# Kernel optimization log

Hardware: AMD Instinct MI355X
Metric: run time of the kernel (lower is better)

Reference implementation:

```python
import jax, jax.numpy as jnp
import numpy as np

N_NODES = 50000


def gcn_conv(x, edge_index, W, b):
    """PyG GCNConv: add self-loops, symmetric deg^{-1/2} norm, W then aggregate."""
    n = x.shape[0]
    loops = jnp.arange(n, dtype=edge_index.dtype)
    src = jnp.concatenate([edge_index[0], loops])  # message sources
    dst = jnp.concatenate([edge_index[1], loops])  # aggregation targets
    h = x @ W  # [N, out_dim] -- transform before gather (PyG order)
    deg = jax.ops.segment_sum(jnp.ones_like(dst, dtype=h.dtype), dst, num_segments=n)
    dinv = jnp.where(deg > 0, jax.lax.rsqrt(jnp.maximum(deg, 1.0)), 0.0)
    norm = dinv[src] * dinv[dst]  # [E+N]
    msg = h[src] * norm[:, None]  # gather + normalize
    out = jax.ops.segment_sum(msg, dst, num_segments=n)  # scatter-add
    return out + b


def setup_inputs() -> dict:
    key = jax.random.key(0)
    k1, k2, k3, k4, k5 = jax.random.split(key, 5)
    N, E, D_IN, D_H, D_OUT = N_NODES, 800000, 128, 256, 16
    x = jax.random.normal(k1, (N, D_IN), dtype=jnp.float32)
    edge_index = jax.random.randint(k2, (2, E), 0, N, dtype=jnp.int64)
    s1 = 1.0 / np.sqrt(D_IN)
    s2 = 1.0 / np.sqrt(D_H)
    W1 = jax.random.uniform(k3, (D_IN, D_H), jnp.float32, -s1, s1)
    b1 = jnp.zeros((D_H,), jnp.float32)
    W2 = jax.random.uniform(k4, (D_H, D_OUT), jnp.float32, -s2, s2)
    b2 = jnp.zeros((D_OUT,), jnp.float32)
    return {"x": x, "edge_index": edge_index, "W1": W1, "b1": b1, "W2": W2, "b2": b2}


def reference(x, edge_index, W1, b1, W2, b2):
    h = jax.nn.relu(gcn_conv(x, edge_index, W1, b1))
    # dropout is identity in eval mode
    logits = gcn_conv(h, edge_index, W2, b2)
    return jax.nn.log_softmax(logits, axis=-1)
```

## Files before the change

### kernel.cpp

```cpp
#include <hip/hip_runtime.h>
#include <math.h>

typedef unsigned int uint;
typedef unsigned short u16;
typedef short short8 __attribute__((ext_vector_type(8)));
typedef float floatx4 __attribute__((ext_vector_type(4)));

union U4S8 { uint4 u; short8 s; };

#define CAPC   64
#define BPB    2048
#define BINCAP 4608


__device__ __forceinline__ float blo(uint u) { return __uint_as_float(u << 16); }
__device__ __forceinline__ float bhi(uint u) { return __uint_as_float(u & 0xffff0000u); }
__device__ __forceinline__ uint pack_bf16(float a, float b) {
    uint ua = __float_as_uint(a), ub = __float_as_uint(b);
    ua = (ua + 0x7fffu + ((ua >> 16) & 1u)) >> 16;
    ub = (ub + 0x7fffu + ((ub >> 16) & 1u)) >> 16;
    return ua | (ub << 16);
}
__device__ __forceinline__ unsigned short rb16(float f) {
    uint u = __float_as_uint(f);
    return (unsigned short)((u + 0x7fffu + ((u >> 16) & 1u)) >> 16);
}
__device__ __forceinline__ int us(short v) { return (int)(unsigned short)v; }

__device__ __forceinline__ int xcd_id() {
    return (int)(__builtin_amdgcn_s_getreg((3 << 11) | 20) & 7);
}


__global__ __launch_bounds__(256) void k_bucket_direct(
    const int* __restrict__ ei, int E, int nblk,
    uint* __restrict__ binctr8, uint* __restrict__ ebin,
    const float* __restrict__ W1, const float* __restrict__ W2,
    uint* __restrict__ W1t, uint* __restrict__ W2t)
{
    __shared__ uint hist[256];
    __shared__ uint off[256];
    int blk = blockIdx.x, tid = threadIdx.x;
    if (blk < nblk) {
        int xcd = xcd_id();
        hist[tid] = 0;
        __syncthreads();
        int base = blk * BPB, end = min(base + BPB, E);
        for (int i = base + tid; i < end; i += 256)
            atomicAdd(&hist[ei[E + i] >> 8], 1u);
        __syncthreads();
        uint h = hist[tid];
        off[tid] = h ? atomicAdd(&binctr8[xcd * 256 + tid], h) : 0u;
        hist[tid] = 0;
        __syncthreads();
        for (int i = base + tid; i < end; i += 256) {
            int sv = ei[i], tv = ei[E + i];
            int bin = tv >> 8;
            uint local = atomicAdd(&hist[bin], 1u);
            uint pos = off[bin] + local;
            if (pos < BINCAP)
                ebin[(size_t)(xcd * 256 + bin) * BINCAP + pos] =
                    ((uint)tv << 16) | (uint)sv;
        }
    } else {
        int i = (blk - nblk) * 256 + tid;
        if (i < 16384) {
            int nn = i >> 6, kd = i & 63;
            W1t[i] = pack_bf16(W1[(size_t)(2 * kd) * 256 + nn], W1[(size_t)(2 * kd + 1) * 256 + nn]);
        } else if (i < 16384 + 2048) {
            int j = i - 16384;
            int o = j >> 7, kd = j & 127;
            W2t[j] = pack_bf16(W2[(size_t)(2 * kd) * 16 + o], W2[(size_t)(2 * kd + 1) * 16 + o]);
        }
    }
}


__global__ __launch_bounds__(256) void k_binbucket(
    const uint* __restrict__ ebin, const uint* __restrict__ binctr8,
    u16* __restrict__ colc, int* __restrict__ degc, float* __restrict__ dinv, int n)
{
    __shared__ uint lbw[64 * 32];
    __shared__ uint lc[64];
    u16* lb = (u16*)lbw;
    int blk = blockIdx.x, tid = threadIdx.x;
    int p = blk >> 2, q = blk & 3;
    int node0 = (p << 8) + (q << 6);

    if (tid < 64) lc[tid] = 0;
    __syncthreads();

    #pragma unroll
    for (int x = 0; x < 8; ++x) {
        uint m = min(binctr8[x * 256 + p], (uint)BINCAP);
        size_t base = (size_t)(x * 256 + p) * BINCAP;
        for (uint i = tid; i < m; i += 256) {
            uint e = ebin[base + i];
            int tl = (int)((e >> 16) & 255u);
            if ((tl >> 6) == q) {
                uint c = atomicAdd(&lc[tl & 63], 1u);
                if (c < (uint)CAPC) lb[(tl & 63) * CAPC + c] = (u16)(e & 0xffffu);
            }
        }
    }
    __syncthreads();

    if (tid < 64) {
        int node = node0 + tid;
        if (node < n) {
            degc[node] = (int)min(lc[tid], (uint)CAPC);
            dinv[node] = rsqrtf((float)lc[tid] + 1.0f);
        }
    }
    uint* colw = (uint*)colc;
    for (int idx = tid; idx < 64 * 32; idx += 256) {
        int nd = node0 + (idx >> 5);
        if (nd < n) colw[(size_t)nd * 32 + (idx & 31)] = lbw[idx];
    }
}


__global__ void k_scale_cast(const float* __restrict__ dinv,
                             const float2* __restrict__ x2,
                             uint* __restrict__ xsb, int total) {
    int j = blockIdx.x * 256 + threadIdx.x;
    if (j >= total) return;
    int row = j >> 6;
    float di = dinv[row];
    float2 v = x2[j];
    xsb[j] = pack_bf16(v.x * di, v.y * di);
}


__global__ __launch_bounds__(256) void k_agg_csr128(
    const int* __restrict__ degc, const u16* __restrict__ colc,
    const float* __restrict__ dinv, const uint* __restrict__ xsb,
    uint* __restrict__ outb, int n)
{
    int node = (blockIdx.x * 256 + threadIdx.x) >> 6;
    int lane = threadIdx.x & 63;
    if (node >= n) return;
    float di = dinv[node];
    int deg = __builtin_amdgcn_readfirstlane(min(degc[node], CAPC));
    const u16* bucket = colc + (size_t)node * CAPC;
    uint u = xsb[(size_t)node * 64 + lane];
    float ax = blo(u), ay = bhi(u);
    for (int j = 0; j < deg; j += 16) {
        U4S8 b0, b1;
        b0.u = *(const uint4*)&bucket[j];
        b1.u = *(const uint4*)&bucket[j + 8];
        uint uu[16];
        #pragma unroll
        for (int k = 0; k < 8; ++k)
            uu[k] = (j + k < deg) ? xsb[(size_t)us(b0.s[k]) * 64 + lane] : 0u;
        #pragma unroll
        for (int k = 0; k < 8; ++k)
            uu[8 + k] = (j + 8 + k < deg) ? xsb[(size_t)us(b1.s[k]) * 64 + lane] : 0u;
        #pragma unroll
        for (int k = 0; k < 16; ++k) { ax += blo(uu[k]); ay += bhi(uu[k]); }
    }
    outb[(size_t)node * 64 + lane] = pack_bf16(ax * di, ay * di);
}


__global__ __launch_bounds__(256) void k_gemm_mfma(
    const uint* __restrict__ Ab,
    const uint* __restrict__ W1t,
    const float* __restrict__ b1,
    const uint* __restrict__ W2t,
    const float* __restrict__ dinv,
    float* __restrict__ H2, int M)
{
    __shared__ uint Alds[64 * 68];
    __shared__ uint Hlds[64 * 132];

    const int t    = threadIdx.x;
    const int mb   = blockIdx.x * 64;
    const int wv   = t >> 6;
    const int lane = t & 63;
    const int c    = lane & 15;
    const int q    = lane >> 4;

    #pragma unroll
    for (int it = 0; it < 4; ++it) {
        int i = it * 256 + t;
        int r = i >> 4, cc = i & 15;
        int gr = mb + r;
        uint4 v = make_uint4(0u, 0u, 0u, 0u);
        if (gr < M) v = ((const uint4*)Ab)[(size_t)gr * 16 + cc];
        *(uint4*)&Alds[r * 68 + cc * 4] = v;
    }
    __syncthreads();

    floatx4 acc[4][4];
    #pragma unroll
    for (int i = 0; i < 4; ++i)
        #pragma unroll
        for (int jj = 0; jj < 4; ++jj) acc[i][jj] = (floatx4)0.f;

    #pragma unroll
    for (int kk = 0; kk < 4; ++kk) {
        U4S8 af[4];
        #pragma unroll
        for (int mt = 0; mt < 4; ++mt)
            af[mt].u = *(const uint4*)&Alds[(mt * 16 + c) * 68 + kk * 16 + q * 4];
        #pragma unroll
        for (int nt = 0; nt < 4; ++nt) {
            int n = wv * 64 + nt * 16 + c;
            U4S8 bf;
            bf.u = ((const uint4*)W1t)[(size_t)n * 16 + kk * 4 + q];
            #pragma unroll
            for (int mt = 0; mt < 4; ++mt)
                acc[mt][nt] = __builtin_amdgcn_mfma_f32_16x16x32_bf16(
                    af[mt].s, bf.s, acc[mt][nt], 0, 0, 0);
        }
    }

    float b1v[4];
    #pragma unroll
    for (int nt = 0; nt < 4; ++nt) b1v[nt] = b1[wv * 64 + nt * 16 + c];

    unsigned short* hs = (unsigned short*)Hlds;
    #pragma unroll
    for (int mt = 0; mt < 4; ++mt)
        #pragma unroll
        for (int nt = 0; nt < 4; ++nt)
            #pragma unroll
            for (int r = 0; r < 4; ++r) {
                float hv = fmaxf(acc[mt][nt][r] + b1v[nt], 0.f);
                int row = mt * 16 + q * 4 + r;
                int colc2 = wv * 64 + nt * 16 + c;
                hs[row * 264 + colc2] = rb16(hv);
            }
    __syncthreads();

    floatx4 acc2 = (floatx4)0.f;
    #pragma unroll
    for (int kk = 0; kk < 8; ++kk) {
        U4S8 av, bv;
        av.u = *(const uint4*)&Hlds[(wv * 16 + c) * 132 + kk * 16 + q * 4];
        bv.u = ((const uint4*)W2t)[(size_t)c * 32 + kk * 4 + q];
        acc2 = __builtin_amdgcn_mfma_f32_16x16x32_bf16(av.s, bv.s, acc2, 0, 0, 0);
    }
    #pragma unroll
    for (int r = 0; r < 4; ++r) {
        int gr = mb + wv * 16 + q * 4 + r;
        if (gr < M) H2[(size_t)gr * 16 + c] = acc2[r] * dinv[gr];
    }
}


__global__ __launch_bounds__(256) void k_agg_csr16_lsm(
    const int* __restrict__ degc, const u16* __restrict__ colc,
    const float* __restrict__ dinv, const float* __restrict__ h2s,
    const float* __restrict__ b2, float* __restrict__ out, int n)
{
    int node = (blockIdx.x * 256 + threadIdx.x) >> 4;
    int lane = threadIdx.x & 15;
    if (node >= n) return;
    float di = dinv[node];
    int deg = min(degc[node], CAPC);
    const u16* bucket = colc + (size_t)node * CAPC;
    float acc = h2s[(size_t)node * 16 + lane];
    for (int j = 0; j < deg; j += 16) {
        U4S8 b0, b1;
        b0.u = *(const uint4*)&bucket[j];
        b1.u = *(const uint4*)&bucket[j + 8];
        float vv[16];
        #pragma unroll
        for (int k = 0; k < 8; ++k)
            vv[k] = (j + k < deg) ? h2s[(size_t)us(b0.s[k]) * 16 + lane] : 0.f;
        #pragma unroll
        for (int k = 0; k < 8; ++k)
            vv[8 + k] = (j + 8 + k < deg) ? h2s[(size_t)us(b1.s[k]) * 16 + lane] : 0.f;
        #pragma unroll
        for (int k = 0; k < 16; ++k) acc += vv[k];
    }
    acc = acc * di + b2[lane];
    float m = acc;
    #pragma unroll
    for (int msk = 1; msk < 16; msk <<= 1) m = fmaxf(m, __shfl_xor(m, msk, 16));
    float ex = __expf(acc - m);
    float ssum = ex;
    #pragma unroll
    for (int msk = 1; msk < 16; msk <<= 1) ssum += __shfl_xor(ssum, msk, 16);
    out[(size_t)node * 16 + lane] = acc - m - __logf(ssum);
}


extern "C" void kernel_launch(void* const* d_in, const int* in_sizes, int n_in,
                              void* d_out, int out_size, void* d_ws, size_t ws_size,
                              hipStream_t stream) {
    const float* x  = (const float*)d_in[0];
    const int*   ei = (const int*)d_in[1];
    const float* W1 = (const float*)d_in[2];
    const float* b1 = (const float*)d_in[3];
    const float* W2 = (const float*)d_in[4];
    const float* b2 = (const float*)d_in[5];
    float* out = (float*)d_out;

    const int N = in_sizes[0] / 128;
    const int E = in_sizes[1] / 2;

    const int NBINS = (N + 255) >> 8;
    const int NBLK  = (E + BPB - 1) / BPB;

    float* ws      = (float*)d_ws;
    float* dinv    = ws;
    int*   degc    = (int*)(ws + 51200);
    uint*  binctr8 = (uint*)(ws + 102400);
    uint*  ebin    = (uint*)(ws + 104448);
    u16*   colc    = (u16*)(ws + 9541632);
    uint*  xsb     = (uint*)(ws + 11141632);
    uint*  aggb    = (uint*)(ws + 14341632);
    float* h2s     = (float*)(ws + 17541632);
    uint*  W1t     = (uint*)(ws + 18341632);
    uint*  W2t     = (uint*)(ws + 18358016);

    hipMemsetAsync(binctr8, 0, 8 * 256 * sizeof(uint), stream);
    k_bucket_direct<<<NBLK + 72, 256, 0, stream>>>(ei, E, NBLK, binctr8, ebin, W1, W2, W1t, W2t);
    k_binbucket <<<NBINS * 4, 256, 0, stream>>>(ebin, binctr8, colc, degc, dinv, N);
    k_scale_cast<<<(N * 64 + 255) / 256, 256, 0, stream>>>(dinv, (const float2*)x, xsb, N * 64);
    k_agg_csr128<<<(N * 64 + 255) / 256, 256, 0, stream>>>(degc, colc, dinv, xsb, aggb, N);
    k_gemm_mfma <<<(N + 63) / 64, 256, 0, stream>>>(aggb, W1t, b1, W2t, dinv, h2s, N);
    k_agg_csr16_lsm<<<(N * 16 + 255) / 256, 256, 0, stream>>>(degc, colc, dinv, h2s, b2, out, N);
}
```

Measured before the change: 166.4 us.

## Split bf16 features into four column slices and aggregate one slice per pass

The scaled bf16 feature matrix is now stored as four contiguous 32-feature slices instead of row-major 128-feature rows. The aggregation kernel is split into four passes, one per slice, with 16 lanes per node, so each pass gathers from a 3.2 MB slice that fits in cache better. The cost is that column indices are re-read four times, 16-lane groups diverge on degree since readfirstlane is dropped, and each gather moves only 64 bytes per neighbor.

```diff
diff --git a/kernel.cpp b/kernel.cpp
--- a/kernel.cpp
+++ b/kernel.cpp
@@ -122,28 +122,34 @@
 
 __global__ void k_scale_cast(const float* __restrict__ dinv,
                              const float2* __restrict__ x2,
-                             uint* __restrict__ xsb, int total) {
+                             uint* __restrict__ xst, int n) {
     int j = blockIdx.x * 256 + threadIdx.x;
-    if (j >= total) return;
-    int row = j >> 6;
+    if (j >= n * 64) return;
+    int row = j >> 6, lane = j & 63;
+    int p = lane >> 4, c = lane & 15;
     float di = dinv[row];
     float2 v = x2[j];
-    xsb[j] = pack_bf16(v.x * di, v.y * di);
-}
-
-
-__global__ __launch_bounds__(256) void k_agg_csr128(
+    xst[(((size_t)p * n + row) << 4) + c] = pack_bf16(v.x * di, v.y * di);
+}
+
+
+__global__ __launch_bounds__(256) void k_agg_chunk(
     const int* __restrict__ degc, const u16* __restrict__ colc,
-    const float* __restrict__ dinv, const uint* __restrict__ xsb,
-    uint* __restrict__ outb, int n)
-{
-    int node = (blockIdx.x * 256 + threadIdx.x) >> 6;
-    int lane = threadIdx.x & 63;
+    const float* __restrict__ dinv, const uint* __restrict__ xst,
+    uint* __restrict__ aggb, int n, int nb_pass)
+{
+    int blk = blockIdx.x, tid = threadIdx.x;
+    int p = blk / nb_pass, rem = blk % nb_pass;
+    int idx = rem * 256 + tid;
+    int node = idx >> 4, lane = idx & 15;
     if (node >= n) return;
+
+    const uint* slice = xst + (((size_t)p * n) << 4);
     float di = dinv[node];
-    int deg = __builtin_amdgcn_readfirstlane(min(degc[node], CAPC));
+    int deg = min(degc[node], CAPC);
     const u16* bucket = colc + (size_t)node * CAPC;
-    uint u = xsb[(size_t)node * 64 + lane];
+
+    uint u = slice[((size_t)node << 4) + lane];
     float ax = blo(u), ay = bhi(u);
     for (int j = 0; j < deg; j += 16) {
         U4S8 b0, b1;
@@ -152,14 +158,14 @@
         uint uu[16];
         #pragma unroll
         for (int k = 0; k < 8; ++k)
-            uu[k] = (j + k < deg) ? xsb[(size_t)us(b0.s[k]) * 64 + lane] : 0u;
+            uu[k] = (j + k < deg) ? slice[((size_t)us(b0.s[k]) << 4) + lane] : 0u;
         #pragma unroll
         for (int k = 0; k < 8; ++k)
-            uu[8 + k] = (j + 8 + k < deg) ? xsb[(size_t)us(b1.s[k]) * 64 + lane] : 0u;
+            uu[8 + k] = (j + 8 + k < deg) ? slice[((size_t)us(b1.s[k]) << 4) + lane] : 0u;
         #pragma unroll
         for (int k = 0; k < 16; ++k) { ax += blo(uu[k]); ay += bhi(uu[k]); }
     }
-    outb[(size_t)node * 64 + lane] = pack_bf16(ax * di, ay * di);
+    aggb[((size_t)node << 6) + (p << 4) + lane] = pack_bf16(ax * di, ay * di);
 }
 
 
@@ -304,6 +310,7 @@
 
     const int NBINS = (N + 255) >> 8;
     const int NBLK  = (E + BPB - 1) / BPB;
+    const int NBP   = (N * 16 + 255) / 256;
 
     float* ws      = (float*)d_ws;
     float* dinv    = ws;
@@ -311,7 +318,7 @@
     uint*  binctr8 = (uint*)(ws + 102400);
     uint*  ebin    = (uint*)(ws + 104448);
     u16*   colc    = (u16*)(ws + 9541632);
-    uint*  xsb     = (uint*)(ws + 11141632);
+    uint*  xst     = (uint*)(ws + 11141632);
     uint*  aggb    = (uint*)(ws + 14341632);
     float* h2s     = (float*)(ws + 17541632);
     uint*  W1t     = (uint*)(ws + 18341632);
@@ -320,8 +327,8 @@
     hipMemsetAsync(binctr8, 0, 8 * 256 * sizeof(uint), stream);
     k_bucket_direct<<<NBLK + 72, 256, 0, stream>>>(ei, E, NBLK, binctr8, ebin, W1, W2, W1t, W2t);
     k_binbucket <<<NBINS * 4, 256, 0, stream>>>(ebin, binctr8, colc, degc, dinv, N);
-    k_scale_cast<<<(N * 64 + 255) / 256, 256, 0, stream>>>(dinv, (const float2*)x, xsb, N * 64);
-    k_agg_csr128<<<(N * 64 + 255) / 256, 256, 0, stream>>>(degc, colc, dinv, xsb, aggb, N);
+    k_scale_cast<<<(N * 64 + 255) / 256, 256, 0, stream>>>(dinv, (const float2*)x, xst, N);
+    k_agg_chunk <<<4 * NBP, 256, 0, stream>>>(degc, colc, dinv, xst, aggb, N, NBP);
     k_gemm_mfma <<<(N + 63) / 64, 256, 0, stream>>>(aggb, W1t, b1, W2t, dinv, h2s, N);
     k_agg_csr16_lsm<<<(N * 16 + 255) / 256, 256, 0, stream>>>(degc, colc, dinv, h2s, b2, out, N);
 }
```

New measurement: 176.7 us. +6.2%, slower.
